# Performance work log

Hardware: AMD Instinct MI355X
Metric: run time of the kernel (lower is better)

The kernel has to match this reference:

```python
import jax, jax.numpy as jnp
import numpy as np

K = 1024       # vq_codebook_size
DC = 64        # vq_code_dim
BETA = 0.25    # commitment cost
DECAY = 0.99   # EMA decay
EPS = 1e-05


def setup_inputs() -> dict:
    key = jax.random.key(0)
    k1, k2, k3 = jax.random.split(key, 3)
    B, H, W = 32, 64, 64
    return {
        "z_e": jax.random.normal(k1, (B, DC, H, W), dtype=jnp.float32),
        "embedding": jax.random.normal(k2, (K, DC), dtype=jnp.float32),
        "cluster_size": jnp.ones((K,), dtype=jnp.float32),
        "embed_avg": jax.random.normal(k3, (K, DC), dtype=jnp.float32),
    }


def reference(z_e, embedding, cluster_size, embed_avg):
    B, D, H, W = z_e.shape
    # flat: [N, D] detached codes, N = B*H*W
    flat = jax.lax.stop_gradient(z_e).transpose(0, 2, 3, 1).reshape(-1, D).astype(jnp.float32)
    distances = ((flat ** 2).sum(1, keepdims=True)
                 + (embedding ** 2).sum(1)
                 - 2.0 * flat @ embedding.T)
    indices = jnp.argmin(distances, axis=-1)          # [N]
    z_q_flat = embedding[indices]                      # gather [N, D]

    # EMA statistics (training path): one-hot sums via segment_sum (scatter-add)
    counts = jax.ops.segment_sum(jnp.ones_like(indices, dtype=jnp.float32), indices, num_segments=K)
    dw = jax.ops.segment_sum(flat, indices, num_segments=K)  # encodings.T @ flat
    new_cluster_size = cluster_size * DECAY + (1.0 - DECAY) * counts
    new_embed_avg = embed_avg * DECAY + (1.0 - DECAY) * dw
    n = new_cluster_size.sum()
    smoothed = (new_cluster_size + EPS) / (n + K * EPS) * n
    new_embedding = new_embed_avg / smoothed[:, None]

    z_q = z_q_flat.reshape(B, H, W, D).transpose(0, 3, 1, 2)  # [B, D, H, W]
    commitment_loss = BETA * jnp.mean((z_e.astype(jnp.float32) - jax.lax.stop_gradient(z_q)) ** 2)
    # straight-through estimator
    z_q_st = z_e + jax.lax.stop_gradient(z_q.astype(z_e.dtype) - z_e)
    return (z_q_st, indices.reshape(B, H, W), commitment_loss,
            new_embedding, new_cluster_size, new_embed_avg)
```

## Files before the change

### kernel.cpp

```cpp
#include <hip/hip_runtime.h>

#define KCB   1024
#define DCV   64
#define HWN   4096
#define CHW   262144
#define NTOT  131072

#define O_ZQ   0
#define O_IDX  8388608
#define O_LOSS 8519680
#define O_NE   8519681
#define O_NCS  8585217
#define O_NEA  8586241

#define W_LOSS  0
#define W_CTR   64
#define W_E2    256
#define W_HLT   4352
#define W_EMBT  266496
#define W_RLIST 528640

#define RCAP   65536
#define MARGIN 0.005f

typedef __attribute__((ext_vector_type(8))) short short8v;
typedef __attribute__((ext_vector_type(4))) float f32x4;

__device__ __forceinline__ unsigned short rne16(float f) {
    unsigned u = __float_as_uint(f);
    unsigned r = (u + 0x7FFFu + ((u >> 16) & 1u)) >> 16;
    return (unsigned short)r;
}

__global__ __launch_bounds__(256) void k_init(
    const float* __restrict__ emb, const float* __restrict__ ea,
    const float* __restrict__ cs, float* __restrict__ out,
    float* __restrict__ e2, short* __restrict__ hl,
    float* __restrict__ embT, double* __restrict__ loss, int* __restrict__ ctr)
{
    int j = blockIdx.x * 256 + threadIdx.x;
    out[O_NEA + j] = 0.99f * ea[j];

    {
        int code = j >> 6, d = j & 63;
        embT[d * KCB + code] = emb[j];
    }
    if (j < KCB) {
        out[O_NCS + j] = 0.99f * cs[j];
        const float* er = emb + j * DCV;
        float s = 0.f;
        #pragma unroll
        for (int d = 0; d < DCV; ++d) { float v = er[d]; s = fmaf(v, v, s); }
        e2[j] = s;
    }
    if (j < 8192) {
        int code = j >> 3, q = j & 7;
        int ch = code >> 6, lc = code & 63;
        const float* src = emb + code * DCV + q * 8;
        short8v h, l;
        #pragma unroll
        for (int t = 0; t < 8; ++t) {
            float x = src[t];
            unsigned short hb = rne16(x);
            float xh = __uint_as_float(((unsigned)hb) << 16);
            h[t] = (short)hb;
            l[t] = (short)rne16(x - xh);
        }
        *(short8v*)(hl + (size_t)(((ch * 2 + 0) * 8 + q) * 64 + lc) * 8) = h;
        *(short8v*)(hl + (size_t)(((ch * 2 + 1) * 8 + q) * 64 + lc) * 8) = l;
    }
    if (j == 0) { *loss = 0.0; *ctr = 0; }
}

__global__ __launch_bounds__(256, 2) void k_dist(
    const float* __restrict__ ze, const char* __restrict__ hl,
    const float* __restrict__ e2g, float* __restrict__ out,
    int* __restrict__ ctr, int* __restrict__ rlist)
{
    __shared__ short lds[2][8192];
    __shared__ float e2s[KCB];

    int tid  = threadIdx.x;
    int lane = tid & 63, w = tid >> 6;
    int g = lane >> 4, c = lane & 15;

    for (int i = tid; i < KCB; i += 256) e2s[i] = e2g[i];

    #define STAGE(buf, ch)                                                     \
        {                                                                      \
            _Pragma("unroll")                                                  \
            for (int r = 0; r < 4; ++r) {                                      \
                int off = (r * 4 + w) * 1024 + lane * 16;                      \
                __builtin_amdgcn_global_load_lds(                              \
                    (const __attribute__((address_space(1))) void*)            \
                        (hl + (size_t)(ch) * 16384 + off),                     \
                    (__attribute__((address_space(3))) void*)                  \
                        ((char*)lds[buf] + off),                               \
                    16, 0, 0);                                                 \
            }                                                                  \
        }

    int rowbase = blockIdx.x * 128 + w * 32;
    short8v ahi[2][2], alo[2][2];
    #pragma unroll
    for (int t = 0; t < 2; ++t) {
        int n = rowbase + t * 16 + c;
        const float* base = ze + (size_t)(n >> 12) * CHW + (n & 4095);
        #pragma unroll
        for (int kh = 0; kh < 2; ++kh) {
            #pragma unroll
            for (int j = 0; j < 8; ++j) {
                int k = kh * 32 + g * 8 + j;
                float x = base[(size_t)k * HWN];
                unsigned short hb = rne16(x);
                float xh = __uint_as_float(((unsigned)hb) << 16);
                ahi[t][kh][j] = (short)hb;
                alo[t][kh][j] = (short)rne16(x - xh);
            }
        }
    }

    float best[8], second[8];
    int   bidx[8];
    #pragma unroll
    for (int i = 0; i < 8; ++i) { best[i] = 3.4e38f; second[i] = 3.4e38f; bidx[i] = 0; }

    STAGE(0, 0);
    __syncthreads();

    int cur = 0;
    for (int ch = 0; ch < 16; ++ch) {
        if (ch < 15) STAGE(cur ^ 1, ch + 1);

        const short* L = lds[cur];
        #pragma unroll
        for (int sub = 0; sub < 4; ++sub) {
            int boff = (sub * 16 + c) * 8;
            short8v bh0 = *(const short8v*)&L[(g * 64) * 8 + boff];
            short8v bh1 = *(const short8v*)&L[((4 + g) * 64) * 8 + boff];
            short8v bl0 = *(const short8v*)&L[((8 + g) * 64) * 8 + boff];
            short8v bl1 = *(const short8v*)&L[((12 + g) * 64) * 8 + boff];

            f32x4 a0 = {0.f, 0.f, 0.f, 0.f}, a1 = {0.f, 0.f, 0.f, 0.f};
            a0 = __builtin_amdgcn_mfma_f32_16x16x32_bf16(ahi[0][0], bh0, a0, 0, 0, 0);
            a1 = __builtin_amdgcn_mfma_f32_16x16x32_bf16(ahi[1][0], bh0, a1, 0, 0, 0);
            a0 = __builtin_amdgcn_mfma_f32_16x16x32_bf16(ahi[0][1], bh1, a0, 0, 0, 0);
            a1 = __builtin_amdgcn_mfma_f32_16x16x32_bf16(ahi[1][1], bh1, a1, 0, 0, 0);
            a0 = __builtin_amdgcn_mfma_f32_16x16x32_bf16(ahi[0][0], bl0, a0, 0, 0, 0);
            a1 = __builtin_amdgcn_mfma_f32_16x16x32_bf16(ahi[1][0], bl0, a1, 0, 0, 0);
            a0 = __builtin_amdgcn_mfma_f32_16x16x32_bf16(ahi[0][1], bl1, a0, 0, 0, 0);
            a1 = __builtin_amdgcn_mfma_f32_16x16x32_bf16(ahi[1][1], bl1, a1, 0, 0, 0);
            a0 = __builtin_amdgcn_mfma_f32_16x16x32_bf16(alo[0][0], bh0, a0, 0, 0, 0);
            a1 = __builtin_amdgcn_mfma_f32_16x16x32_bf16(alo[1][0], bh0, a1, 0, 0, 0);
            a0 = __builtin_amdgcn_mfma_f32_16x16x32_bf16(alo[0][1], bh1, a0, 0, 0, 0);
            a1 = __builtin_amdgcn_mfma_f32_16x16x32_bf16(alo[1][1], bh1, a1, 0, 0, 0);

            float e2v = e2s[ch * 64 + sub * 16 + c];
            int  code = ch * 64 + sub * 16 + c;
            #pragma unroll
            for (int t = 0; t < 2; ++t) {
                f32x4 av = t ? a1 : a0;
                #pragma unroll
                for (int r = 0; r < 4; ++r) {
                    int i = t * 4 + r;
                    float s = fmaf(-2.f, av[r], e2v);
                    bool lb = s < best[i];
                    second[i] = fminf(second[i], fmaxf(best[i], s));
                    best[i]   = fminf(best[i], s);
                    bidx[i]   = lb ? code : bidx[i];
                }
            }
        }
        __syncthreads();
        cur ^= 1;
    }

    #pragma unroll
    for (int i = 0; i < 8; ++i) {
        float b = best[i], s2 = second[i];
        int bi = bidx[i];
        #pragma unroll
        for (int m = 1; m < 16; m <<= 1) {
            float ob = __shfl_xor(b, m, 64);
            float os = __shfl_xor(s2, m, 64);
            int   oi = __shfl_xor(bi, m, 64);
            float ns = fminf(fmaxf(b, ob), fminf(s2, os));
            bi = (ob < b || (ob == b && oi < bi)) ? oi : bi;
            b  = fminf(b, ob);
            s2 = ns;
        }
        if (c == 0) {
            int t = i >> 2, r = i & 3;
            int n = rowbase + t * 16 + g * 4 + r;
            out[O_IDX + n] = (float)bi;
            if (s2 - b < MARGIN) {
                int p = atomicAdd(ctr, 1);
                if (p < RCAP) rlist[p] = n;
            }
        }
    }
    #undef STAGE
}

__global__ __launch_bounds__(256) void k_refine(
    const float* __restrict__ ze, const float* __restrict__ emb,
    float* __restrict__ out, const int* __restrict__ ctr,
    const int* __restrict__ rlist)
{
    int lane = threadIdx.x & 63;
    int gw   = (blockIdx.x * blockDim.x + threadIdx.x) >> 6;
    int nw   = (gridDim.x * blockDim.x) >> 6;
    int cnt  = *ctr;
    if (cnt > RCAP) cnt = RCAP;

    for (int i = gw; i < cnt; i += nw) {
        int n = rlist[i];
        const float* zp = ze + (size_t)(n >> 12) * CHW + (n & 4095);
        float x[DCV];
        #pragma unroll
        for (int d = 0; d < DCV; ++d) x[d] = zp[(size_t)d * HWN];

        double bd = 1e300;
        int    bi = 0;
        #pragma unroll 1
        for (int cc = 0; cc < KCB / 64; ++cc) {
            int k = cc * 64 + lane;
            const float4* eb4 = (const float4*)(emb + k * DCV);
            double a0 = 0.0, a1 = 0.0;
            #pragma unroll
            for (int q = 0; q < DCV / 4; ++q) {
                float4 v = eb4[q];
                double d0 = (double)x[q * 4 + 0] - (double)v.x;
                double d1 = (double)x[q * 4 + 1] - (double)v.y;
                double d2 = (double)x[q * 4 + 2] - (double)v.z;
                double d3 = (double)x[q * 4 + 3] - (double)v.w;
                a0 = fma(d0, d0, a0); a1 = fma(d1, d1, a1);
                a0 = fma(d2, d2, a0); a1 = fma(d3, d3, a1);
            }
            double dist = a0 + a1;
            if (dist < bd || (dist == bd && k < bi)) { bd = dist; bi = k; }
        }
        #pragma unroll
        for (int off = 32; off > 0; off >>= 1) {
            double od = __shfl_xor(bd, off, 64);
            int    oi = __shfl_xor(bi, off, 64);
            if (od < bd || (od == bd && oi < bi)) { bd = od; bi = oi; }
        }
        if (lane == 0) out[O_IDX + n] = (float)bi;
    }
}

__global__ __launch_bounds__(256) void k_post(
    const float* __restrict__ ze, const float* __restrict__ embT,
    float* __restrict__ out, double* __restrict__ loss)
{
    int gidx = blockIdx.x >> 5, b = blockIdx.x & 31;
    __shared__ float acc[8 * KCB];
    __shared__ float cnt[KCB];
    __shared__ float wsum[4];
    for (int i = threadIdx.x; i < 8 * KCB; i += 256) acc[i] = 0.f;
    if (gidx == 0) for (int i = threadIdx.x; i < KCB; i += 256) cnt[i] = 0.f;
    __syncthreads();

    const float* zp  = ze  + (size_t)b * CHW + (size_t)gidx * 8 * HWN;
    float*       zq  = out + O_ZQ + (size_t)b * CHW + (size_t)gidx * 8 * HWN;
    const float* ipf = out + O_IDX + b * HWN;
    const float* eT  = embT + (size_t)gidx * 8 * KCB;

    float lp = 0.f;
    for (int hw = threadIdx.x; hw < HWN; hw += 256) {
        int idx = (int)ipf[hw];
        #pragma unroll
        for (int i = 0; i < 8; ++i) {
            float x = zp[(size_t)i * HWN + hw];
            float e = eT[i * KCB + idx];
            float df = x - e;
            lp = fmaf(df, df, lp);
            zq[(size_t)i * HWN + hw] = x + (e - x);
            atomicAdd(&acc[idx * 8 + i], x);
        }
        if (gidx == 0) atomicAdd(&cnt[idx], 1.f);
    }

    #pragma unroll
    for (int off = 32; off > 0; off >>= 1) lp += __shfl_down(lp, off, 64);
    int lane = threadIdx.x & 63, wid = threadIdx.x >> 6;
    if (lane == 0) wsum[wid] = lp;
    __syncthreads();
    if (threadIdx.x == 0) {
        double s = (double)wsum[0] + wsum[1] + wsum[2] + wsum[3];
        atomicAdd(loss, s);
    }

    for (int j = threadIdx.x; j < 8192; j += 256) {
        float v = acc[j];
        if (v != 0.f) atomicAdd(&out[O_NEA + (j >> 3) * DCV + gidx * 8 + (j & 7)], 0.01f * v);
    }
    if (gidx == 0)
        for (int k = threadIdx.x; k < KCB; k += 256) {
            float cv = cnt[k];
            if (cv != 0.f) atomicAdd(&out[O_NCS + k], 0.01f * cv);
        }
}

__global__ __launch_bounds__(256) void k_fin(
    float* __restrict__ out, const double* __restrict__ loss)
{
    __shared__ float red[4];
    int t = threadIdx.x;
    float s = 0.f;
    #pragma unroll
    for (int q = 0; q < 4; ++q) s += out[O_NCS + t * 4 + q];
    #pragma unroll
    for (int off = 32; off > 0; off >>= 1) s += __shfl_down(s, off, 64);
    int lane = t & 63, wid = t >> 6;
    if (lane == 0) red[wid] = s;
    __syncthreads();
    float n = red[0] + red[1] + red[2] + red[3];

    int j = blockIdx.x * 256 + t;
    int k = j >> 6;
    float ncs = out[O_NCS + k];
    float sm = (ncs + 1e-5f) / (n + (float)KCB * 1e-5f) * n;
    out[O_NE + j] = out[O_NEA + j] / sm;

    if (blockIdx.x == 0 && t == 0)
        out[O_LOSS] = (float)(0.25 * (*loss) / (double)(NTOT * DCV));
}

extern "C" void kernel_launch(void* const* d_in, const int* in_sizes, int n_in,
                              void* d_out, int out_size, void* d_ws, size_t ws_size,
                              hipStream_t stream)
{
    const float* ze  = (const float*)d_in[0];
    const float* emb = (const float*)d_in[1];
    const float* cs  = (const float*)d_in[2];
    const float* ea  = (const float*)d_in[3];
    float* out = (float*)d_out;

    char*   w     = (char*)d_ws;
    double* loss  = (double*)(w + W_LOSS);
    int*    ctr   = (int*)(w + W_CTR);
    float*  e2    = (float*)(w + W_E2);
    short*  hl    = (short*)(w + W_HLT);
    float*  embT  = (float*)(w + W_EMBT);
    int*    rlist = (int*)(w + W_RLIST);

    k_init  <<<256, 256, 0, stream>>>(emb, ea, cs, out, e2, hl, embT, loss, ctr);
    k_dist  <<<1024, 256, 0, stream>>>(ze, (const char*)hl, e2, out, ctr, rlist);
    k_refine<<<256, 256, 0, stream>>>(ze, emb, out, ctr, rlist);
    k_post  <<<256, 256, 0, stream>>>(ze, embT, out, loss);
    k_fin   <<<256, 256, 0, stream>>>(out, loss);
}
```

Measured before the change: 238.4 us.

## Switch split-precision distance MFMA from bf16 to scaled fp16 and tighten refine margin

Replaces the bf16 hi/lo split of inputs and codebook with an fp16 hi part plus a residual scaled by 2048. The hi and correction products go into separate accumulators, which are combined before the distance update. The more accurate split lets the near-tie margin drop from 0.005 to 1e-3, so fewer rows should land on the refine list. It also reads codebook norms directly from global memory instead of staging them in LDS, computes those norms in double, and changes the shared accumulator layout in the post kernel to code-major per dimension, which may reduce atomic bank conflicts. Risks include fp16 overflow or underflow on large or tiny values and extra scalar work in the inner loop.

```diff
diff --git a/kernel.cpp b/kernel.cpp
--- a/kernel.cpp
+++ b/kernel.cpp
@@ -21,21 +21,15 @@
 #define W_RLIST 528640
 
 #define RCAP   65536
-#define MARGIN 0.005f
-
-typedef __attribute__((ext_vector_type(8))) short short8v;
+#define MARGIN 1e-3f
+
+typedef __attribute__((ext_vector_type(8))) _Float16 half8v;
 typedef __attribute__((ext_vector_type(4))) float f32x4;
-
-__device__ __forceinline__ unsigned short rne16(float f) {
-    unsigned u = __float_as_uint(f);
-    unsigned r = (u + 0x7FFFu + ((u >> 16) & 1u)) >> 16;
-    return (unsigned short)r;
-}
 
 __global__ __launch_bounds__(256) void k_init(
     const float* __restrict__ emb, const float* __restrict__ ea,
     const float* __restrict__ cs, float* __restrict__ out,
-    float* __restrict__ e2, short* __restrict__ hl,
+    float* __restrict__ e2, _Float16* __restrict__ hl,
     float* __restrict__ embT, double* __restrict__ loss, int* __restrict__ ctr)
 {
     int j = blockIdx.x * 256 + threadIdx.x;
@@ -48,26 +42,25 @@
     if (j < KCB) {
         out[O_NCS + j] = 0.99f * cs[j];
         const float* er = emb + j * DCV;
-        float s = 0.f;
-        #pragma unroll
-        for (int d = 0; d < DCV; ++d) { float v = er[d]; s = fmaf(v, v, s); }
-        e2[j] = s;
+        double s = 0.0;
+        #pragma unroll
+        for (int d = 0; d < DCV; ++d) { double v = (double)er[d]; s += v * v; }
+        e2[j] = (float)s;
     }
     if (j < 8192) {
         int code = j >> 3, q = j & 7;
         int ch = code >> 6, lc = code & 63;
         const float* src = emb + code * DCV + q * 8;
-        short8v h, l;
+        half8v h, l;
         #pragma unroll
         for (int t = 0; t < 8; ++t) {
             float x = src[t];
-            unsigned short hb = rne16(x);
-            float xh = __uint_as_float(((unsigned)hb) << 16);
-            h[t] = (short)hb;
-            l[t] = (short)rne16(x - xh);
-        }
-        *(short8v*)(hl + (size_t)(((ch * 2 + 0) * 8 + q) * 64 + lc) * 8) = h;
-        *(short8v*)(hl + (size_t)(((ch * 2 + 1) * 8 + q) * 64 + lc) * 8) = l;
+            _Float16 hx = (_Float16)x;
+            h[t] = hx;
+            l[t] = (_Float16)((x - (float)hx) * 2048.0f);
+        }
+        *(half8v*)(hl + (size_t)(((ch * 2 + 0) * 8 + q) * 64 + lc) * 8) = h;
+        *(half8v*)(hl + (size_t)(((ch * 2 + 1) * 8 + q) * 64 + lc) * 8) = l;
     }
     if (j == 0) { *loss = 0.0; *ctr = 0; }
 }
@@ -77,14 +70,11 @@
     const float* __restrict__ e2g, float* __restrict__ out,
     int* __restrict__ ctr, int* __restrict__ rlist)
 {
-    __shared__ short lds[2][8192];
-    __shared__ float e2s[KCB];
+    __shared__ _Float16 lds[2][8192];
 
     int tid  = threadIdx.x;
     int lane = tid & 63, w = tid >> 6;
     int g = lane >> 4, c = lane & 15;
-
-    for (int i = tid; i < KCB; i += 256) e2s[i] = e2g[i];
 
     #define STAGE(buf, ch)                                                     \
         {                                                                      \
@@ -101,7 +91,7 @@
         }
 
     int rowbase = blockIdx.x * 128 + w * 32;
-    short8v ahi[2][2], alo[2][2];
+    half8v ahi[2][2], alo[2][2];
     #pragma unroll
     for (int t = 0; t < 2; ++t) {
         int n = rowbase + t * 16 + c;
@@ -112,10 +102,9 @@
             for (int j = 0; j < 8; ++j) {
                 int k = kh * 32 + g * 8 + j;
                 float x = base[(size_t)k * HWN];
-                unsigned short hb = rne16(x);
-                float xh = __uint_as_float(((unsigned)hb) << 16);
-                ahi[t][kh][j] = (short)hb;
-                alo[t][kh][j] = (short)rne16(x - xh);
+                _Float16 hx = (_Float16)x;
+                ahi[t][kh][j] = hx;
+                alo[t][kh][j] = (_Float16)((x - (float)hx) * 2048.0f);
             }
         }
     }
@@ -132,38 +121,41 @@
     for (int ch = 0; ch < 16; ++ch) {
         if (ch < 15) STAGE(cur ^ 1, ch + 1);
 
-        const short* L = lds[cur];
+        const _Float16* L = lds[cur];
         #pragma unroll
         for (int sub = 0; sub < 4; ++sub) {
             int boff = (sub * 16 + c) * 8;
-            short8v bh0 = *(const short8v*)&L[(g * 64) * 8 + boff];
-            short8v bh1 = *(const short8v*)&L[((4 + g) * 64) * 8 + boff];
-            short8v bl0 = *(const short8v*)&L[((8 + g) * 64) * 8 + boff];
-            short8v bl1 = *(const short8v*)&L[((12 + g) * 64) * 8 + boff];
-
-            f32x4 a0 = {0.f, 0.f, 0.f, 0.f}, a1 = {0.f, 0.f, 0.f, 0.f};
-            a0 = __builtin_amdgcn_mfma_f32_16x16x32_bf16(ahi[0][0], bh0, a0, 0, 0, 0);
-            a1 = __builtin_amdgcn_mfma_f32_16x16x32_bf16(ahi[1][0], bh0, a1, 0, 0, 0);
-            a0 = __builtin_amdgcn_mfma_f32_16x16x32_bf16(ahi[0][1], bh1, a0, 0, 0, 0);
-            a1 = __builtin_amdgcn_mfma_f32_16x16x32_bf16(ahi[1][1], bh1, a1, 0, 0, 0);
-            a0 = __builtin_amdgcn_mfma_f32_16x16x32_bf16(ahi[0][0], bl0, a0, 0, 0, 0);
-            a1 = __builtin_amdgcn_mfma_f32_16x16x32_bf16(ahi[1][0], bl0, a1, 0, 0, 0);
-            a0 = __builtin_amdgcn_mfma_f32_16x16x32_bf16(ahi[0][1], bl1, a0, 0, 0, 0);
-            a1 = __builtin_amdgcn_mfma_f32_16x16x32_bf16(ahi[1][1], bl1, a1, 0, 0, 0);
-            a0 = __builtin_amdgcn_mfma_f32_16x16x32_bf16(alo[0][0], bh0, a0, 0, 0, 0);
-            a1 = __builtin_amdgcn_mfma_f32_16x16x32_bf16(alo[1][0], bh0, a1, 0, 0, 0);
-            a0 = __builtin_amdgcn_mfma_f32_16x16x32_bf16(alo[0][1], bh1, a0, 0, 0, 0);
-            a1 = __builtin_amdgcn_mfma_f32_16x16x32_bf16(alo[1][1], bh1, a1, 0, 0, 0);
-
-            float e2v = e2s[ch * 64 + sub * 16 + c];
+            half8v bh0 = *(const half8v*)&L[(g * 64) * 8 + boff];
+            half8v bh1 = *(const half8v*)&L[((4 + g) * 64) * 8 + boff];
+            half8v bl0 = *(const half8v*)&L[((8 + g) * 64) * 8 + boff];
+            half8v bl1 = *(const half8v*)&L[((12 + g) * 64) * 8 + boff];
+
+            f32x4 a0h = {0.f, 0.f, 0.f, 0.f}, a1h = {0.f, 0.f, 0.f, 0.f};
+            f32x4 a0c = {0.f, 0.f, 0.f, 0.f}, a1c = {0.f, 0.f, 0.f, 0.f};
+            a0h = __builtin_amdgcn_mfma_f32_16x16x32_f16(ahi[0][0], bh0, a0h, 0, 0, 0);
+            a1h = __builtin_amdgcn_mfma_f32_16x16x32_f16(ahi[1][0], bh0, a1h, 0, 0, 0);
+            a0h = __builtin_amdgcn_mfma_f32_16x16x32_f16(ahi[0][1], bh1, a0h, 0, 0, 0);
+            a1h = __builtin_amdgcn_mfma_f32_16x16x32_f16(ahi[1][1], bh1, a1h, 0, 0, 0);
+            a0c = __builtin_amdgcn_mfma_f32_16x16x32_f16(ahi[0][0], bl0, a0c, 0, 0, 0);
+            a1c = __builtin_amdgcn_mfma_f32_16x16x32_f16(ahi[1][0], bl0, a1c, 0, 0, 0);
+            a0c = __builtin_amdgcn_mfma_f32_16x16x32_f16(ahi[0][1], bl1, a0c, 0, 0, 0);
+            a1c = __builtin_amdgcn_mfma_f32_16x16x32_f16(ahi[1][1], bl1, a1c, 0, 0, 0);
+            a0c = __builtin_amdgcn_mfma_f32_16x16x32_f16(alo[0][0], bh0, a0c, 0, 0, 0);
+            a1c = __builtin_amdgcn_mfma_f32_16x16x32_f16(alo[1][0], bh0, a1c, 0, 0, 0);
+            a0c = __builtin_amdgcn_mfma_f32_16x16x32_f16(alo[0][1], bh1, a0c, 0, 0, 0);
+            a1c = __builtin_amdgcn_mfma_f32_16x16x32_f16(alo[1][1], bh1, a1c, 0, 0, 0);
+
+            float e2v = e2g[ch * 64 + sub * 16 + c];
             int  code = ch * 64 + sub * 16 + c;
             #pragma unroll
             for (int t = 0; t < 2; ++t) {
-                f32x4 av = t ? a1 : a0;
+                f32x4 avh = t ? a1h : a0h;
+                f32x4 avc = t ? a1c : a0c;
                 #pragma unroll
                 for (int r = 0; r < 4; ++r) {
                     int i = t * 4 + r;
-                    float s = fmaf(-2.f, av[r], e2v);
+                    float dotv = fmaf(avc[r], 4.8828125e-4f, avh[r]);
+                    float s = fmaf(-2.f, dotv, e2v);
                     bool lb = s < best[i];
                     second[i] = fminf(second[i], fmaxf(best[i], s));
                     best[i]   = fminf(best[i], s);
@@ -277,7 +269,7 @@
             float df = x - e;
             lp = fmaf(df, df, lp);
             zq[(size_t)i * HWN + hw] = x + (e - x);
-            atomicAdd(&acc[idx * 8 + i], x);
+            atomicAdd(&acc[i * KCB + idx], x);
         }
         if (gidx == 0) atomicAdd(&cnt[idx], 1.f);
     }
@@ -294,7 +286,8 @@
 
     for (int j = threadIdx.x; j < 8192; j += 256) {
         float v = acc[j];
-        if (v != 0.f) atomicAdd(&out[O_NEA + (j >> 3) * DCV + gidx * 8 + (j & 7)], 0.01f * v);
+        if (v != 0.f)
+            atomicAdd(&out[O_NEA + (j & 1023) * DCV + gidx * 8 + (j >> 10)], 0.01f * v);
     }
     if (gidx == 0)
         for (int k = threadIdx.x; k < KCB; k += 256) {
@@ -338,13 +331,13 @@
     const float* ea  = (const float*)d_in[3];
     float* out = (float*)d_out;
 
-    char*   w     = (char*)d_ws;
-    double* loss  = (double*)(w + W_LOSS);
-    int*    ctr   = (int*)(w + W_CTR);
-    float*  e2    = (float*)(w + W_E2);
-    short*  hl    = (short*)(w + W_HLT);
-    float*  embT  = (float*)(w + W_EMBT);
-    int*    rlist = (int*)(w + W_RLIST);
+    char*     w     = (char*)d_ws;
+    double*   loss  = (double*)(w + W_LOSS);
+    int*      ctr   = (int*)(w + W_CTR);
+    float*    e2    = (float*)(w + W_E2);
+    _Float16* hl    = (_Float16*)(w + W_HLT);
+    float*    embT  = (float*)(w + W_EMBT);
+    int*      rlist = (int*)(w + W_RLIST);
 
     k_init  <<<256, 256, 0, stream>>>(emb, ea, cs, out, e2, hl, embT, loss, ctr);
     k_dist  <<<1024, 256, 0, stream>>>(ze, (const char*)hl, e2, out, ctr, rlist);
```

Result: slower. 315.2 us (+32.2%).
